# Kernel tuning notes

Measured on AMD Instinct MI355X. Metric: run time of the kernel, lower is better.

## Reference

```python
import jax, jax.numpy as jnp
import numpy as np

MAX_SHIFT = 20
DAILY_CYCLE = 288
HORIZON_OFFSET = 1


def _valid_shifts(T):
    shifts = sorted(set(list(range(-MAX_SHIFT, 1)) + [-(DAILY_CYCLE - HORIZON_OFFSET)]))
    return [s for s in shifts if 0 < abs(s) < T]


def setup_inputs() -> dict:
    key = jax.random.key(0)
    k1, k2 = jax.random.split(key)
    x = jax.random.normal(k1, (2, 320, 207, 64), dtype=jnp.float32)
    w = jax.random.normal(k2, (1, 1), dtype=jnp.float32)  # LearnableSimilarity linear weight
    return {"x": x, "w": w}


def reference(x, w):
    B, T, L, D = x.shape
    shifts = _valid_shifts(T)
    S = len(shifts)  # 21 for T=320

    # Build zero-padded shifted copies: for s<0, shifted[:, t] = x[:, t+|s|] (zeros at tail).
    sh_list = []
    for s in shifts:
        p = abs(s)
        pad = jnp.zeros((B, p, L, D), dtype=x.dtype)
        if s < 0:
            sh_list.append(jnp.concatenate([x[:, p:], pad], axis=1))
        else:
            sh_list.append(jnp.concatenate([pad, x[:, :-p]], axis=1))
    xs = jnp.stack(sh_list, axis=1)  # [B, S, T, L, D]

    # Learnable similarity = (x . y) * w; mean over T fused into the einsum.
    wscalar = w[0, 0]
    sim_avg = jnp.einsum('btld,bstmd->bslm', x, xs) * (wscalar / T)  # [B,S,L,L]  l=target, m=shifted

    # Faithful to original: softmax over joint (S*target-L) axis, then raw reshape to (L, S*L).
    flat = sim_avg.reshape(B, S * L, L)
    soft = jax.nn.softmax(flat, axis=1)
    attn = soft.reshape(B, L, S * L)  # NOTE: reshape, not transpose (matches torch .view)

    x_flat = xs.transpose(0, 2, 1, 3, 4).reshape(B, T, S * L, D)  # m index = s*L + link
    out = jnp.einsum('btmd,blm->btld', x_flat, attn)  # [B,T,L,D]
    return out
```

## Files before the change

kernel.cpp:

```cpp
#include <hip/hip_runtime.h>
#include <hip/hip_bf16.h>

#define B_DIM 2
#define T_DIM 320
#define L_DIM 207
#define D_DIM 64
#define S_DIM 21
#define J_TOT (S_DIM * L_DIM)
#define MPAD 224
#define IPAD 256
#define NSPLIT 4
#define TSPLIT 80
#define NCH_A 128
#define CH_A 34
#define NCH_P 128
#define CH_P 34
#define LD_ROW (L_DIM * D_DIM)
#define SLAB_B 26496

typedef __attribute__((ext_vector_type(8))) short bf16x8;
typedef __attribute__((ext_vector_type(4))) float f32x4;

__device__ inline unsigned short f2bf(float f) {
    unsigned int u = __builtin_bit_cast(unsigned int, f);
    u = (u + 0x7FFFu + ((u >> 16) & 1u)) >> 16;
    return (unsigned short)u;
}

__device__ inline int shift_p(int s) { return (s == 0) ? 287 : (21 - s); }
__device__ inline int imin(int a, int b) { return a < b ? a : b; }
__device__ inline int imax(int a, int b) { return a > b ? a : b; }

__device__ __forceinline__ void glds16(const void* g, void* l) {
    __builtin_amdgcn_global_load_lds(
        (const __attribute__((address_space(1))) void*)g,
        (__attribute__((address_space(3))) void*)l,
        16, 0, 0);
}

__global__ void __launch_bounds__(256) k_prep(const float* __restrict__ x,
                                              unsigned short* __restrict__ xbf,
                                              unsigned short* __restrict__ xt) {
    __shared__ float tile[L_DIM * 66];
    int bt = blockIdx.x;
    const float* src = x + (size_t)bt * LD_ROW;
    int tid = threadIdx.x;
    for (int idx = tid; idx < L_DIM * D_DIM; idx += 256) {
        int l = idx >> 6, d = idx & 63;
        tile[l * 66 + d] = src[idx];
    }
    __syncthreads();
    unsigned short* dst1 = xbf + (size_t)bt * LD_ROW;
    for (int idx = tid; idx < L_DIM * D_DIM; idx += 256) {
        int l = idx >> 6, d = idx & 63;
        dst1[idx] = f2bf(tile[l * 66 + d]);
    }
    unsigned short* dst2 = xt + (size_t)bt * (7 * 64 * 32);
    if (tid < MPAD) {
        int mc = tid >> 5, mi = tid & 31;
        for (int d = 0; d < D_DIM; ++d) {
            float v = (tid < L_DIM) ? tile[tid * 66 + d] : 0.0f;
            dst2[(mc * 64 + d) * 32 + mi] = f2bf(v);
        }
    }
}

__global__ void __launch_bounds__(512, 2) k_simr(const unsigned short* __restrict__ xbf,
                                                 const unsigned short* __restrict__ zpage,
                                                 float* __restrict__ part) {
    __shared__ __align__(16) unsigned short Asl[8][2048];
    __shared__ __align__(16) unsigned short Bsl[24][2048];

    int id = blockIdx.x;
    int split = id / 98;
    int r2 = id % 98;
    int b = r2 & 1;
    int pb = r2 >> 1;
    int lfb = pb / 7, mfb = pb % 7;

    int t0 = split * TSPLIT;
    int t1 = t0 + TSPLIT;

    int tid = threadIdx.x;
    int w = tid >> 6, lane = tid & 63;
    int wl = w & 1, wm = (w >> 1) & 1, h = w >> 2;
    int fr = lane & 15, kg = lane >> 4;
    int x7 = fr & 7;

    int lf = lfb * 2 + wl;
    int mf = mfb * 2 + wm;
    bool wvalid = (lf <= 12) && (mf <= 12);

    bool isA = (w < 4);
    int gq = (w & 3) * 64 + lane;
    int grow = gq >> 3, gc = gq & 7;
    int srcoff = grow * 128 + ((gc ^ (grow & 7)) * 16);
    int dstoff = (w & 3) * 1024;

    const char* xb = (const char*)xbf;
    size_t abase = (size_t)b * T_DIM * SLAB_B + lfb * 4096;
    size_t bbase = (size_t)b * T_DIM * SLAB_B + mfb * 4096;

    int lrA = wl * 16 + fr, lrB = wm * 16 + fr;
    int c0 = ((0 + kg) ^ x7) * 16, c1 = ((4 + kg) ^ x7) * 16;
    int aoff0 = lrA * 128 + c0, aoff1 = lrA * 128 + c1;
    int boff0 = lrB * 128 + c0, boff1 = lrB * 128 + c1;

    f32x4 acc[10];
#pragma unroll
    for (int j = 0; j < 10; ++j) acc[j] = f32x4{0.f, 0.f, 0.f, 0.f};
    bf16x8 ring[10][2];

    if (isA) {
#pragma unroll
        for (int i = 0; i < 3; ++i)
            glds16(xb + abase + (size_t)(t0 + i) * SLAB_B + srcoff,
                   (char*)Asl[(t0 + i) & 7] + dstoff);
    } else {
        for (int k = 1; k <= 22; ++k) {
            int tau = t0 + k;
            const char* src = (tau < T_DIM) ? (xb + bbase + (size_t)tau * SLAB_B) : (const char*)zpage;
            glds16(src + srcoff, (char*)Bsl[tau % 24] + dstoff);
        }
    }
    asm volatile("s_waitcnt vmcnt(0)" ::: "memory");
    __builtin_amdgcn_s_barrier();
    asm volatile("" ::: "memory");
    if (wvalid) {
#pragma unroll
        for (int j = 1; j <= 9; ++j) {
            int tau = t0 + 20 - 10 * h - j;
            const char* sb = (const char*)Bsl[tau % 24];
            ring[10 - j][0] = *(const bf16x8*)(sb + boff0);
            ring[10 - j][1] = *(const bf16x8*)(sb + boff1);
        }
    }

    for (int tb = t0; tb < t1; tb += 10) {
#pragma unroll
        for (int u = 0; u < 10; ++u) {
            int t = tb + u;
            if (isA) {
                int tn = t + 3;
                const char* src = (tn < T_DIM) ? (xb + abase + (size_t)tn * SLAB_B) : (const char*)zpage;
                glds16(src + srcoff, (char*)Asl[tn & 7] + dstoff);
            } else {
                int tau = t + 23;
                const char* src = (tau < T_DIM) ? (xb + bbase + (size_t)tau * SLAB_B) : (const char*)zpage;
                glds16(src + srcoff, (char*)Bsl[tau % 24] + dstoff);
            }
            asm volatile("s_waitcnt vmcnt(3)" ::: "memory");
            __builtin_amdgcn_s_barrier();
            asm volatile("" ::: "memory");
            if (wvalid) {
                const char* sa = (const char*)Asl[t & 7];
                bf16x8 a0 = *(const bf16x8*)(sa + aoff0);
                bf16x8 a1 = *(const bf16x8*)(sa + aoff1);
                int tauf = t + 20 - 10 * h;
                const char* sb = (const char*)Bsl[tauf % 24];
                ring[u][0] = *(const bf16x8*)(sb + boff0);
                ring[u][1] = *(const bf16x8*)(sb + boff1);
#pragma unroll
                for (int j = 0; j < 10; ++j) {
                    acc[j] = __builtin_amdgcn_mfma_f32_16x16x32_bf16(a0, ring[(u - j + 10) % 10][0], acc[j], 0, 0, 0);
                    acc[j] = __builtin_amdgcn_mfma_f32_16x16x32_bf16(a1, ring[(u - j + 10) % 10][1], acc[j], 0, 0, 0);
                }
            }
        }
    }

    int col = mf * 16 + fr;
    if (col < L_DIM) {
        float* pbase = part + (size_t)(split * B_DIM + b) * J_TOT * L_DIM;
#pragma unroll
        for (int j = 0; j < 10; ++j) {
            int s = 10 * h + 1 + j;
#pragma unroll
            for (int r = 0; r < 4; ++r) {
                int row = lf * 16 + kg * 4 + r;
                if (row < L_DIM)
                    pbase[((size_t)s * L_DIM + row) * L_DIM + col] = acc[j][r];
            }
        }
    }
}

__global__ void __launch_bounds__(256) k_sim0(const unsigned short* __restrict__ xbf,
                                              float* __restrict__ part) {
    __shared__ __align__(16) unsigned short S[2][2][8192];

    int id = blockIdx.x;
    int tile = id & 3;
    int rest = id >> 2;
    int split = rest & 3;
    int b = rest >> 2;
    int l0 = (tile >> 1) * 128, m0 = (tile & 1) * 128;

    const int p = 287;
    int nt = T_DIM - p;
    int t0 = (split * nt) >> 2;
    int t1 = (((split + 1) * nt) >> 2);

    int tid = threadIdx.x;
    int wave = tid >> 6, lane = tid & 63;
    int wl = wave >> 1, wm = wave & 1;
    int fr = lane & 15, kg = lane >> 4;
    int x7 = fr & 7;

    int rN = 0, cN = 0;
#pragma unroll
    for (int g = 0; g < 4; ++g) {
        if (l0 + (g * 2 + wl) * 16 < L_DIM) rN = g + 1;
        if (m0 + (g * 2 + wm) * 16 < L_DIM) cN = g + 1;
    }

    int srcoff[4];
#pragma unroll
    for (int i = 0; i < 4; ++i) {
        int n = i * 256 + wave * 64 + lane;
        int row = n >> 3, c = n & 7;
        srcoff[i] = row * 128 + ((c ^ (row & 7)) * 16);
    }
    int wbase = wave * 1024;

    int cb0 = (kg ^ x7) * 16, cb1 = ((4 + kg) ^ x7) * 16;
    int aro[4], bro[4];
#pragma unroll
    for (int g = 0; g < 4; ++g) {
        aro[g] = ((g * 2 + wl) * 16 + fr) * 128;
        bro[g] = ((g * 2 + wm) * 16 + fr) * 128;
    }

    f32x4 acc[4][4];
#pragma unroll
    for (int i = 0; i < 4; ++i)
#pragma unroll
        for (int j = 0; j < 4; ++j) acc[i][j] = f32x4{0.f, 0.f, 0.f, 0.f};

    const size_t LDB = (size_t)LD_ROW * 2;
    const char* abase = (const char*)xbf + ((size_t)b * T_DIM * LD_ROW + (size_t)l0 * 64) * 2;
    const char* bbase = (const char*)xbf + ((size_t)(b * T_DIM + p) * LD_ROW + (size_t)m0 * 64) * 2;

    if (t1 > t0) {
        {
            const char* a = abase + (size_t)t0 * LDB;
            const char* bb = bbase + (size_t)t0 * LDB;
            char* lA = (char*)&S[0][0][0] + wbase;
            char* lB = (char*)&S[0][1][0] + wbase;
#pragma unroll
            for (int i = 0; i < 4; ++i) {
                glds16(a + srcoff[i], lA + i * 4096);
                glds16(bb + srcoff[i], lB + i * 4096);
            }
        }
        int cur = 0;
        for (int t = t0; t < t1; ++t) {
            bool more = (t + 1 < t1);
            if (more) {
                const char* a = abase + (size_t)(t + 1) * LDB;
                const char* bb = bbase + (size_t)(t + 1) * LDB;
                char* lA = (char*)&S[cur ^ 1][0][0] + wbase;
                char* lB = (char*)&S[cur ^ 1][1][0] + wbase;
#pragma unroll
                for (int i = 0; i < 4; ++i) {
                    glds16(a + srcoff[i], lA + i * 4096);
                    glds16(bb + srcoff[i], lB + i * 4096);
                }
                asm volatile("s_waitcnt vmcnt(8)" ::: "memory");
            } else {
                asm volatile("s_waitcnt vmcnt(0)" ::: "memory");
            }
            __builtin_amdgcn_s_barrier();
            asm volatile("" ::: "memory");
            const char* lA = (const char*)&S[cur][0][0];
            const char* lB = (const char*)&S[cur][1][0];
#pragma unroll
            for (int kd = 0; kd < 2; ++kd) {
                int cb = kd ? cb1 : cb0;
                bf16x8 af[4], bv[4];
#pragma unroll
                for (int g = 0; g < 4; ++g)
                    if (g < rN) af[g] = *(const bf16x8*)(lA + aro[g] + cb);
#pragma unroll
                for (int g = 0; g < 4; ++g)
                    if (g < cN) bv[g] = *(const bf16x8*)(lB + bro[g] + cb);
#pragma unroll
                for (int rg = 0; rg < 4; ++rg)
                    if (rg < rN)
#pragma unroll
                        for (int cg = 0; cg < 4; ++cg)
                            if (cg < cN)
                                acc[rg][cg] = __builtin_amdgcn_mfma_f32_16x16x32_bf16(
                                    af[rg], bv[cg], acc[rg][cg], 0, 0, 0);
            }
            asm volatile("" ::: "memory");
            __builtin_amdgcn_s_barrier();
            cur ^= 1;
        }
    }

    float* pdst = part + ((size_t)(split * B_DIM + b) * J_TOT + (size_t)0 * L_DIM) * L_DIM;
#pragma unroll
    for (int rg = 0; rg < 4; ++rg)
#pragma unroll
        for (int cg = 0; cg < 4; ++cg) {
            int col = m0 + (cg * 2 + wm) * 16 + fr;
            if (col < L_DIM) {
#pragma unroll
                for (int r = 0; r < 4; ++r) {
                    int row = l0 + (rg * 2 + wl) * 16 + kg * 4 + r;
                    if (row < L_DIM) pdst[(size_t)row * L_DIM + col] = acc[rg][cg][r];
                }
            }
        }
}

__global__ void __launch_bounds__(256) k_sumexp(const float* __restrict__ part,
                                                const float* __restrict__ w,
                                                float* __restrict__ psum) {
    int c = blockIdx.x, b = blockIdx.y;
    int m = threadIdx.x;
    if (m >= L_DIM) return;
    float scale = w[0] / (float)T_DIM;
    int j0 = c * CH_A, j1 = imin(j0 + CH_A, J_TOT);
    float acc = 0.0f;
    for (int j = j0; j < j1; ++j) {
        float v = 0.0f;
#pragma unroll
        for (int r = 0; r < NSPLIT; ++r)
            v += part[((size_t)(r * B_DIM + b) * J_TOT + j) * L_DIM + m];
        acc += __expf(v * scale);
    }
    psum[(b * NCH_A + c) * L_DIM + m] = acc;
}

__global__ void __launch_bounds__(256) k_pack(const float* __restrict__ part,
                                              const float* __restrict__ w,
                                              const float* __restrict__ psum,
                                              unsigned short* __restrict__ pp) {
    __shared__ float sinv[L_DIM];
    int c = blockIdx.x, b = blockIdx.y;
    int tid = threadIdx.x;
    if (tid < L_DIM) {
        float g = 0.0f;
        for (int q = 0; q < NCH_A; ++q) g += psum[(b * NCH_A + q) * L_DIM + tid];
        sinv[tid] = 1.0f / g;
    }
    __syncthreads();
    if (tid >= MPAD) return;
    float scale = w[0] / (float)T_DIM;
    float inv = (tid < L_DIM) ? sinv[tid] : 0.0f;
    int mc = tid >> 5, mi = tid & 31;
    int j0 = c * CH_P, j1 = imin(j0 + CH_P, J_TOT);
    for (int j = j0; j < j1; ++j) {
        float pr = 0.0f;
        if (tid < L_DIM) {
            float v = 0.0f;
#pragma unroll
            for (int r = 0; r < NSPLIT; ++r)
                v += part[((size_t)(r * B_DIM + b) * J_TOT + j) * L_DIM + tid];
            pr = __expf(v * scale) * inv;
        }
        int i = j / S_DIM, s = j % S_DIM;
        pp[((((size_t)b * S_DIM + s) * 7 + mc) * IPAD + i) * 32 + mi] = f2bf(pr);
    }
}

__global__ void __launch_bounds__(256) k_out(const unsigned short* __restrict__ ppn,
                                             const unsigned short* __restrict__ xtn,
                                             float* __restrict__ out) {
    __shared__ __align__(16) unsigned short As[4][128 * 32];
    __shared__ __align__(16) unsigned short Bs[4][2][64 * 32];

    int id = blockIdx.x;
    int low = id & 7;
    int b = low >> 2, tr = low & 3;
    int rest = id >> 3;
    int tg = rest >> 1;
    int ih = rest & 1;
    int t0 = tr * TSPLIT + tg * 2;
    int i0 = ih * 128;

    int tid = threadIdx.x;
    int wave = tid >> 6, lane = tid & 63;
    int wt = wave >> 1, wi = wave & 1;
    int fr = lane & 15, kg = lane >> 4;
    int t = t0 + wt;

    const char* ppb = (const char*)ppn + (size_t)b * (S_DIM * 7 * IPAD * 32) * 2;
    const char* xtb = (const char*)xtn + (size_t)b * (T_DIM * 7 * 64 * 32) * 2;

    int asrc[2], bsrc[2];
#pragma unroll
    for (int i = 0; i < 2; ++i) {
        int n = wave * 128 + i * 64 + lane;
        int row = n >> 2, c = n & 3;
        asrc[i] = row * 64 + ((c ^ ((row >> 1) & 3)) * 16);
        int n2 = (wave & 1) * 128 + i * 64 + lane;
        int row2 = n2 >> 2, c2 = n2 & 3;
        bsrc[i] = row2 * 64 + ((c2 ^ ((row2 >> 1) & 3)) * 16);
    }
    int btau = wave >> 1;

    int cb = (kg ^ ((fr >> 1) & 3)) * 16;
    int aro[4], bro[4];
#pragma unroll
    for (int g = 0; g < 4; ++g) {
        aro[g] = (wi * 64 + g * 16 + fr) * 64;
        bro[g] = (g * 16 + fr) * 64;
    }

    f32x4 acc[4][4];
#pragma unroll
    for (int i = 0; i < 4; ++i)
#pragma unroll
        for (int j = 0; j < 4; ++j) acc[i][j] = f32x4{0.f, 0.f, 0.f, 0.f};

    int has0 = (t0 <= 32) ? 1 : 0;
    int sBegin = imax(1, t0 - 298);
    int ns = (21 - sBegin) + has0;
    int Q = ns * 7;

    auto sOf = [&](int k) { return (has0 && k == 0) ? 0 : sBegin + (k - has0); };

    auto stage = [&](int q, int buf) {
        int ss = sOf(q / 7), mc = q % 7;
        const char* ga = ppb + (((size_t)(ss * 7 + mc) * IPAD + i0) * 32) * 2;
        char* lA = (char*)&As[buf][0] + wave * 2048;
        glds16(ga + asrc[0], lA);
        glds16(ga + asrc[1], lA + 1024);
        int pp_ = shift_p(ss);
        int tau = imin(t0 + btau + pp_, T_DIM - 1);
        const char* gb = xtb + ((size_t)tau * 7 + mc) * 4096;
        char* lB = (char*)&Bs[buf][btau][0] + (wave & 1) * 2048;
        glds16(gb + bsrc[0], lB);
        glds16(gb + bsrc[1], lB + 1024);
    };

    stage(0, 0);
    stage(1, 1);
    for (int q = 0; q < Q; ++q) {
        if (q + 2 < Q) {
            stage(q + 2, (q + 2) & 3);
            asm volatile("s_waitcnt vmcnt(8)" ::: "memory");
        } else if (q + 1 < Q) {
            asm volatile("s_waitcnt vmcnt(4)" ::: "memory");
        } else {
            asm volatile("s_waitcnt vmcnt(0)" ::: "memory");
        }
        __builtin_amdgcn_s_barrier();
        asm volatile("" ::: "memory");
        int sc = sOf(q / 7);
        int p = shift_p(sc);
        if (t + p < T_DIM) {
            const char* lA = (const char*)&As[q & 3][0];
            const char* lB = (const char*)&Bs[q & 3][wt][0];
            bf16x8 af[4], bv[4];
#pragma unroll
            for (int g = 0; g < 4; ++g) af[g] = *(const bf16x8*)(lA + aro[g] + cb);
#pragma unroll
            for (int g = 0; g < 4; ++g) bv[g] = *(const bf16x8*)(lB + bro[g] + cb);
#pragma unroll
            for (int rg = 0; rg < 4; ++rg)
#pragma unroll
                for (int cg = 0; cg < 4; ++cg)
                    acc[rg][cg] = __builtin_amdgcn_mfma_f32_16x16x32_bf16(
                        af[rg], bv[cg], acc[rg][cg], 0, 0, 0);
        }
        asm volatile("" ::: "memory");
    }

    float* obase = out + (size_t)(b * T_DIM + t) * LD_ROW;
#pragma unroll
    for (int rg = 0; rg < 4; ++rg)
#pragma unroll
        for (int cg = 0; cg < 4; ++cg) {
            int d = cg * 16 + fr;
#pragma unroll
            for (int r = 0; r < 4; ++r) {
                int i = i0 + wi * 64 + rg * 16 + kg * 4 + r;
                if (i < L_DIM) obase[(size_t)i * D_DIM + d] = acc[rg][cg][r];
            }
        }
}

extern "C" void kernel_launch(void* const* d_in, const int* in_sizes, int n_in,
                              void* d_out, int out_size, void* d_ws, size_t ws_size,
                              hipStream_t stream) {
    const float* x = (const float*)d_in[0];
    const float* w = (const float*)d_in[1];
    float* out = (float*)d_out;

    char* ws = (char*)d_ws;
    size_t off = 0;
    auto carve = [&](size_t bytes) {
        void* p = ws + off;
        off += (bytes + 255) & ~(size_t)255;
        return p;
    };
    unsigned short* xbf = (unsigned short*)carve((size_t)B_DIM * T_DIM * LD_ROW * 2);
    unsigned short* xt  = (unsigned short*)carve((size_t)B_DIM * T_DIM * 7 * 64 * 32 * 2);
    float* part         = (float*)carve((size_t)NSPLIT * B_DIM * J_TOT * L_DIM * 4);
    float* psum         = (float*)carve((size_t)B_DIM * NCH_A * L_DIM * 4);
    size_t pp_bytes = (size_t)B_DIM * S_DIM * 7 * IPAD * 32 * 2;
    unsigned short* pp  = (unsigned short*)carve(pp_bytes);
    unsigned short* zpage = (unsigned short*)carve(4096);

    k_prep<<<B_DIM * T_DIM, 256, 0, stream>>>(x, xbf, xt);
    hipMemsetAsync(zpage, 0, 4096, stream);
    k_simr<<<NSPLIT * 98, 512, 0, stream>>>(xbf, zpage, part);
    k_sim0<<<B_DIM * NSPLIT * 4, 256, 0, stream>>>(xbf, part);
    k_sumexp<<<dim3(NCH_A, B_DIM), 256, 0, stream>>>(part, w, psum);
    hipMemsetAsync(pp, 0, pp_bytes, stream);
    k_pack<<<dim3(NCH_P, B_DIM), 256, 0, stream>>>(part, w, psum, pp);
    k_out<<<640, 256, 0, stream>>>(pp, xt, out);
}
```

Baseline: 399.4 us.

## Load B operand directly to registers, double-buffer A, skip padded row tiles

```diff
diff --git a/kernel.cpp b/kernel.cpp
--- a/kernel.cpp
+++ b/kernel.cpp
@@ -369,8 +369,7 @@
 __global__ void __launch_bounds__(256) k_out(const unsigned short* __restrict__ ppn,
                                              const unsigned short* __restrict__ xtn,
                                              float* __restrict__ out) {
-    __shared__ __align__(16) unsigned short As[4][128 * 32];
-    __shared__ __align__(16) unsigned short Bs[4][2][64 * 32];
+    __shared__ __align__(16) unsigned short As[2][128 * 32];
 
     int id = blockIdx.x;
     int low = id & 7;
@@ -390,25 +389,27 @@
     const char* ppb = (const char*)ppn + (size_t)b * (S_DIM * 7 * IPAD * 32) * 2;
     const char* xtb = (const char*)xtn + (size_t)b * (T_DIM * 7 * 64 * 32) * 2;
 
-    int asrc[2], bsrc[2];
+    int asrc[2];
 #pragma unroll
     for (int i = 0; i < 2; ++i) {
         int n = wave * 128 + i * 64 + lane;
         int row = n >> 2, c = n & 3;
         asrc[i] = row * 64 + ((c ^ ((row >> 1) & 3)) * 16);
-        int n2 = (wave & 1) * 128 + i * 64 + lane;
-        int row2 = n2 >> 2, c2 = n2 & 3;
-        bsrc[i] = row2 * 64 + ((c2 ^ ((row2 >> 1) & 3)) * 16);
-    }
-    int btau = wave >> 1;
+    }
 
     int cb = (kg ^ ((fr >> 1) & 3)) * 16;
-    int aro[4], bro[4];
+    int aro[4];
+    int rN = 0;
 #pragma unroll
     for (int g = 0; g < 4; ++g) {
-        aro[g] = (wi * 64 + g * 16 + fr) * 64;
-        bro[g] = (g * 16 + fr) * 64;
-    }
+        aro[g] = ((g * 2 + wi) * 16 + fr) * 64;
+        if (i0 + (g * 2 + wi) * 16 < L_DIM) rN = g + 1;
+    }
+
+    int boff0 = ((0 * 16 + fr) * 32 + kg * 8) * 2;
+    int boff1 = ((1 * 16 + fr) * 32 + kg * 8) * 2;
+    int boff2 = ((2 * 16 + fr) * 32 + kg * 8) * 2;
+    int boff3 = ((3 * 16 + fr) * 32 + kg * 8) * 2;
 
     f32x4 acc[4][4];
 #pragma unroll
@@ -423,28 +424,35 @@
 
     auto sOf = [&](int k) { return (has0 && k == 0) ? 0 : sBegin + (k - has0); };
 
-    auto stage = [&](int q, int buf) {
+    auto stageA = [&](int q, int buf) {
         int ss = sOf(q / 7), mc = q % 7;
         const char* ga = ppb + (((size_t)(ss * 7 + mc) * IPAD + i0) * 32) * 2;
         char* lA = (char*)&As[buf][0] + wave * 2048;
         glds16(ga + asrc[0], lA);
         glds16(ga + asrc[1], lA + 1024);
+    };
+
+    bf16x8 bn0, bn1, bn2, bn3, bc0, bc1, bc2, bc3;
+    auto loadB = [&](int q) {
+        int ss = sOf(q / 7), mc = q % 7;
         int pp_ = shift_p(ss);
-        int tau = imin(t0 + btau + pp_, T_DIM - 1);
-        const char* gb = xtb + ((size_t)tau * 7 + mc) * 4096;
-        char* lB = (char*)&Bs[buf][btau][0] + (wave & 1) * 2048;
-        glds16(gb + bsrc[0], lB);
-        glds16(gb + bsrc[1], lB + 1024);
+        int tau = imin(t + pp_, T_DIM - 1);
+        const char* gb = xtb + (size_t)(tau * 7 + mc) * 4096;
+        bn0 = *(const bf16x8*)(gb + boff0);
+        bn1 = *(const bf16x8*)(gb + boff1);
+        bn2 = *(const bf16x8*)(gb + boff2);
+        bn3 = *(const bf16x8*)(gb + boff3);
     };
 
-    stage(0, 0);
-    stage(1, 1);
+    stageA(0, 0);
+    loadB(0);
+    int cur = 0;
     for (int q = 0; q < Q; ++q) {
-        if (q + 2 < Q) {
-            stage(q + 2, (q + 2) & 3);
-            asm volatile("s_waitcnt vmcnt(8)" ::: "memory");
-        } else if (q + 1 < Q) {
-            asm volatile("s_waitcnt vmcnt(4)" ::: "memory");
+        bc0 = bn0; bc1 = bn1; bc2 = bn2; bc3 = bn3;
+        if (q + 1 < Q) {
+            stageA(q + 1, cur ^ 1);
+            loadB(q + 1);
+            asm volatile("s_waitcnt vmcnt(6)" ::: "memory");
         } else {
             asm volatile("s_waitcnt vmcnt(0)" ::: "memory");
         }
@@ -453,21 +461,23 @@
         int sc = sOf(q / 7);
         int p = shift_p(sc);
         if (t + p < T_DIM) {
-            const char* lA = (const char*)&As[q & 3][0];
-            const char* lB = (const char*)&Bs[q & 3][wt][0];
-            bf16x8 af[4], bv[4];
-#pragma unroll
-            for (int g = 0; g < 4; ++g) af[g] = *(const bf16x8*)(lA + aro[g] + cb);
-#pragma unroll
-            for (int g = 0; g < 4; ++g) bv[g] = *(const bf16x8*)(lB + bro[g] + cb);
+            const char* lA = (const char*)&As[cur][0];
+            bf16x8 af[4];
+#pragma unroll
+            for (int g = 0; g < 4; ++g)
+                if (g < rN) af[g] = *(const bf16x8*)(lA + aro[g] + cb);
 #pragma unroll
             for (int rg = 0; rg < 4; ++rg)
-#pragma unroll
-                for (int cg = 0; cg < 4; ++cg)
-                    acc[rg][cg] = __builtin_amdgcn_mfma_f32_16x16x32_bf16(
-                        af[rg], bv[cg], acc[rg][cg], 0, 0, 0);
+                if (rg < rN) {
+                    acc[rg][0] = __builtin_amdgcn_mfma_f32_16x16x32_bf16(af[rg], bc0, acc[rg][0], 0, 0, 0);
+                    acc[rg][1] = __builtin_amdgcn_mfma_f32_16x16x32_bf16(af[rg], bc1, acc[rg][1], 0, 0, 0);
+                    acc[rg][2] = __builtin_amdgcn_mfma_f32_16x16x32_bf16(af[rg], bc2, acc[rg][2], 0, 0, 0);
+                    acc[rg][3] = __builtin_amdgcn_mfma_f32_16x16x32_bf16(af[rg], bc3, acc[rg][3], 0, 0, 0);
+                }
         }
         asm volatile("" ::: "memory");
+        __builtin_amdgcn_s_barrier();
+        cur ^= 1;
     }
 
     float* obase = out + (size_t)(b * T_DIM + t) * LD_ROW;
@@ -478,7 +488,7 @@
             int d = cg * 16 + fr;
 #pragma unroll
             for (int r = 0; r < 4; ++r) {
-                int i = i0 + wi * 64 + rg * 16 + kg * 4 + r;
+                int i = i0 + (rg * 2 + wi) * 16 + kg * 4 + r;
                 if (i < L_DIM) obase[(size_t)i * D_DIM + d] = acc[rg][cg][r];
             }
         }
```

Measured after the change: 349.6 us. 12.5% less time.
